# Optimization experiments

Measured on AMD Instinct MI355X. Metric: run time of the kernel, lower is better.

The kernel has to match this reference:

```python
import jax, jax.numpy as jnp
import numpy as np

B, N, C, H = 2, 2048, 1024, 16
D = C // H  # head_dim = 64


def setup_inputs() -> dict:
    key = jax.random.key(0)
    ks = jax.random.split(key, 5)
    s = 1.0 / np.sqrt(C)
    return {
        "q": jax.random.normal(ks[0], (B, N, C), dtype=jnp.float32),
        "W_qkv": jax.random.normal(ks[1], (C, 3 * C), dtype=jnp.float32) * s,
        "b_qkv": jnp.zeros((3 * C,), dtype=jnp.float32),
        "W_proj": jax.random.normal(ks[2], (C, C), dtype=jnp.float32) * s,
        "b_proj": jnp.zeros((C,), dtype=jnp.float32),
    }


def reference(q, W_qkv, b_qkv, W_proj, b_proj):
    # Self-attention: k = v = q. Full 3C projection (as in the torch code).
    qkv = q @ W_qkv + b_qkv  # [B, N, 3C]
    qh = qkv[:, :, :C].reshape(B, N, H, D)
    kh = qkv[:, :, C:2 * C].reshape(B, N, H, D)
    vh = qkv[:, :, 2 * C:].reshape(B, N, H, D)
    scale = D ** -0.5
    # [B, H, N, N] attention logits
    attn = jnp.einsum("bnhd,bmhd->bhnm", qh, kh) * scale
    attn = jax.nn.softmax(attn, axis=-1)
    out = jnp.einsum("bhnm,bmhd->bnhd", attn, vh).reshape(B, N, C)
    return out @ W_proj + b_proj
```

## Files before the change

kernel.cpp:

```cpp
#include <hip/hip_runtime.h>
#include <stdint.h>

typedef __bf16 bf16_t;
typedef __bf16 bf16x8 __attribute__((ext_vector_type(8)));
typedef __bf16 bf16x4 __attribute__((ext_vector_type(4)));
typedef float f32x4 __attribute__((ext_vector_type(4)));

#define L2E 1.44269504088896340736f
#define QSCALE (0.125f * L2E)

__device__ __forceinline__ void gload16(const bf16_t* g, bf16_t* l) {
  __builtin_amdgcn_global_load_lds(
      (const __attribute__((address_space(1))) void*)g,
      (__attribute__((address_space(3))) void*)l, 16, 0, 0);
}

__device__ __forceinline__ float fexp2(float x) {
  float r;
  asm("v_exp_f32 %0, %1" : "=v"(r) : "v"(x));
  return r;
}

__global__ __launch_bounds__(256) void cast_q_kernel(const float* __restrict__ in,
                                                     bf16_t* __restrict__ out) {
  int i = blockIdx.x * 256 + threadIdx.x;
  float4 v = reinterpret_cast<const float4*>(in)[i];
  bf16x4 o;
  o[0] = (bf16_t)v.x; o[1] = (bf16_t)v.y; o[2] = (bf16_t)v.z; o[3] = (bf16_t)v.w;
  reinterpret_cast<bf16x4*>(out)[i] = o;
}

__global__ __launch_bounds__(256) void transpose_cast_kernel(const float* __restrict__ in,
                                                             bf16_t* __restrict__ out,
                                                             int K, int N) {
  __shared__ float tile[64][65];
  int k0 = blockIdx.y * 64, n0 = blockIdx.x * 64;
  int t = threadIdx.x;
  int r = t >> 4, c4 = (t & 15) * 4;
#pragma unroll
  for (int rr = 0; rr < 4; rr++) {
    int row = r + rr * 16;
    float4 v = *reinterpret_cast<const float4*>(&in[(size_t)(k0 + row) * N + n0 + c4]);
    tile[row][c4 + 0] = v.x; tile[row][c4 + 1] = v.y;
    tile[row][c4 + 2] = v.z; tile[row][c4 + 3] = v.w;
  }
  __syncthreads();
#pragma unroll
  for (int rr = 0; rr < 4; rr++) {
    int nr = r + rr * 16;
    bf16x4 o;
#pragma unroll
    for (int i = 0; i < 4; i++) o[i] = (bf16_t)tile[c4 + i][nr];
    *reinterpret_cast<bf16x4*>(&out[(size_t)(n0 + nr) * K + k0 + c4]) = o;
  }
}

template <int MODE, int BM>
__global__ __launch_bounds__(256) void gemm_kernel(const bf16_t* __restrict__ A,
                                                   const bf16_t* __restrict__ Bt,
                                                   const float* __restrict__ bias,
                                                   void* __restrict__ out,
                                                   bf16_t* __restrict__ vT,
                                                   int K, int gm, int gn, int ldo) {
  constexpr int ACH = BM / 8;
  constexpr int NCH = ACH + 16;
  constexpr int CPW = NCH / 4;
  constexpr int IR = BM / 32;
  constexpr int SMEM = (MODE == 0) ? 17408 : (BM * 64 + 8192);
  __shared__ __align__(16) bf16_t smem[SMEM];
  bf16_t* At = smem;
  bf16_t* Bts = smem + BM * 64;
  const int t = threadIdx.x, lane = t & 63, w = t >> 6;
  const int g = lane >> 4, q = lane & 15;
  const int bid = blockIdx.x, x = bid & 7, r = bid >> 3;
  const int qm = gm >> 2, qn = gn >> 1;
  const int lm = r % qm, ln = r / qm;
  const int m0 = ((x & 3) * qm + lm) * BM, n0 = ((x >> 2) * qn + ln) * 128;
  const int wm = (w >> 1) * (BM / 2), wn = (w & 1) * 64;

  const bf16_t* srcp[CPW]; int dsto[CPW];
#pragma unroll
  for (int i = 0; i < CPW; i++) {
    int cI = i * 4 + w;
    bool isA = cI < ACH;
    int row = (isA ? cI : cI - ACH) * 8 + (lane >> 3);
    int p = (lane & 7) ^ (row & 7);
    srcp[i] = (isA ? A + (size_t)(m0 + row) * K : Bt + (size_t)(n0 + row) * K) + p * 8;
    dsto[i] = (isA ? cI * 512 : BM * 64 + (cI - ACH) * 512);
  }

  f32x4 acc[IR][4];
#pragma unroll
  for (int i = 0; i < IR; i++)
#pragma unroll
    for (int j = 0; j < 4; j++) acc[i][j] = (f32x4){0.f, 0.f, 0.f, 0.f};

  for (int k0 = 0; k0 < K; k0 += 64) {
    __syncthreads();
#pragma unroll
    for (int i = 0; i < CPW; i++) gload16(srcp[i] + k0, &smem[dsto[i]]);
    __syncthreads();
#pragma unroll
    for (int dc = 0; dc < 2; dc++) {
      bf16x8 am[IR], bn[4];
#pragma unroll
      for (int i = 0; i < IR; i++) {
        int ra = wm + 16 * i + q;
        am[i] = *reinterpret_cast<const bf16x8*>(&At[ra * 64 + ((dc * 32 + g * 8) ^ ((ra & 7) * 8))]);
      }
#pragma unroll
      for (int j = 0; j < 4; j++) {
        int rb = wn + 16 * j + q;
        bn[j] = *reinterpret_cast<const bf16x8*>(&Bts[rb * 64 + ((dc * 32 + g * 8) ^ ((rb & 7) * 8))]);
      }
#pragma unroll
      for (int i = 0; i < IR; i++)
#pragma unroll
        for (int j = 0; j < 4; j++)
          acc[i][j] = __builtin_amdgcn_mfma_f32_16x16x32_bf16(am[i], bn[j], acc[i][j], 0, 0, 0);
    }
  }

  if (MODE == 0 && n0 >= 2048) {
    __syncthreads();
    bf16_t* TT = smem;
#pragma unroll
    for (int i = 0; i < IR; i++)
#pragma unroll
      for (int j = 0; j < 4; j++)
#pragma unroll
        for (int rr = 0; rr < 4; rr++) {
          int ch = wn + 16 * j + q;
          int tok = wm + 16 * i + 4 * g + rr;
          float v = acc[i][j][rr] + bias[n0 + ch];
          TT[ch * 136 + (((tok >> 3) ^ (ch & 7)) * 8) + (tok & 7)] = (bf16_t)v;
        }
    __syncthreads();
    const int bb = m0 >> 11;
    const int t0 = m0 & 2047;
#pragma unroll
    for (int it = 0; it < 8; it++) {
      int ch = it * 16 + w * 4 + (lane >> 4);
      int ck = lane & 15;
      uint4 val = *reinterpret_cast<const uint4*>(&TT[ch * 136 + ((ck ^ (ch & 7)) * 8)]);
      int vch = (n0 - 2048) + ch;
      bf16_t* dst = vT + ((size_t)(bb * 16 + (vch >> 6)) * 64 + (vch & 63)) * 2048 + t0 + ck * 8;
      *reinterpret_cast<uint4*>(dst) = val;
    }
  } else {
#pragma unroll
    for (int i = 0; i < IR; i++)
#pragma unroll
      for (int j = 0; j < 4; j++)
#pragma unroll
        for (int rr = 0; rr < 4; rr++) {
          int row = m0 + wm + 16 * i + 4 * g + rr;
          int col = n0 + wn + 16 * j + q;
          float v = acc[i][j][rr] + bias[col];
          if (MODE == 0) {
            if (col < 1024) v *= QSCALE;
            ((bf16_t*)out)[(size_t)row * ldo + col] = (bf16_t)v;
          } else {
            ((float*)out)[(size_t)row * ldo + col] = v;
          }
        }
  }
}

__global__ __launch_bounds__(256) void attn_kernel(const bf16_t* __restrict__ qk,
                                                   const bf16_t* __restrict__ vT,
                                                   bf16_t* __restrict__ aout) {
  __shared__ __align__(16) bf16_t sK[2][4096];
  __shared__ __align__(16) bf16_t sV[2][4096];
  __shared__ __align__(16) bf16_t sP[4][1024];

  const int t = threadIdx.x, lane = t & 63, w = t >> 6;
  const int g = lane >> 4, q = lane & 15;
  const int bid = blockIdx.x, xr = bid >> 3;
  const int bh = (bid & 7) * 4 + (xr >> 5);
  const int b = bh >> 4, h = bh & 15;
  const int q0 = (xr & 31) * 64 + w * 16;
  const bf16_t* qk_b = qk + (size_t)b * 2048 * 2048;
  const bf16_t* vT_h = vT + (size_t)bh * 64 * 2048;
  bf16_t* Pw = sP[w];

  const bf16_t* srcK[2]; const bf16_t* srcV[2]; int dsto[2];
#pragma unroll
  for (int i = 0; i < 2; i++) {
    int gI = (w * 2 + i) * 64 + lane;
    int row = gI >> 3, p = (gI & 7) ^ (row & 7);
    srcK[i] = qk_b + (size_t)row * 2048 + 1024 + h * 64 + p * 8;
    srcV[i] = vT_h + (size_t)row * 2048 + p * 8;
    dsto[i] = (w * 2 + i) * 512;
  }

  bf16x8 bq[2];
  {
    const bf16_t* qr = qk_b + (size_t)(q0 + q) * 2048 + h * 64;
    bq[0] = *reinterpret_cast<const bf16x8*>(qr + g * 8);
    bq[1] = *reinterpret_cast<const bf16x8*>(qr + 32 + g * 8);
  }

  bf16x8 ones;
#pragma unroll
  for (int i = 0; i < 8; i++) ones[i] = (bf16_t)1.0f;

  f32x4 oacc[4];
#pragma unroll
  for (int c = 0; c < 4; c++) oacc[c] = (f32x4){0.f, 0.f, 0.f, 0.f};
  f32x4 lacc = (f32x4){0.f, 0.f, 0.f, 0.f};

#pragma unroll
  for (int i = 0; i < 2; i++) {
    gload16(srcK[i], &sK[0][dsto[i]]);
    gload16(srcV[i], &sV[0][dsto[i]]);
  }
  __syncthreads();

  for (int tt = 0; tt < 32; tt++) {
    const int cur = tt & 1;
    if (tt + 1 < 32) {
      size_t koffK = (size_t)(tt + 1) * 64 * 2048;
      size_t koffV = (size_t)(tt + 1) * 64;
#pragma unroll
      for (int i = 0; i < 2; i++) {
        gload16(srcK[i] + koffK, &sK[cur ^ 1][dsto[i]]);
        gload16(srcV[i] + koffV, &sV[cur ^ 1][dsto[i]]);
      }
    }

    const bf16_t* Kc = sK[cur];
    f32x4 s[4];
#pragma unroll
    for (int c = 0; c < 4; c++) {
      int row = 16 * c + q, sw = (q & 7) * 8;
      bf16x8 ka0 = *reinterpret_cast<const bf16x8*>(&Kc[row * 64 + ((g * 8) ^ sw)]);
      bf16x8 ka1 = *reinterpret_cast<const bf16x8*>(&Kc[row * 64 + ((32 + g * 8) ^ sw)]);
      f32x4 z = (f32x4){0.f, 0.f, 0.f, 0.f};
      z = __builtin_amdgcn_mfma_f32_16x16x32_bf16(ka0, bq[0], z, 0, 0, 0);
      z = __builtin_amdgcn_mfma_f32_16x16x32_bf16(ka1, bq[1], z, 0, 0, 0);
      s[c] = z;
    }

#pragma unroll
    for (int c = 0; c < 4; c++) {
      bf16x4 pk;
#pragma unroll
      for (int rr = 0; rr < 4; rr++) pk[rr] = (bf16_t)fexp2(s[c][rr]);
      *reinterpret_cast<bf16x4*>(
          &Pw[q * 64 + (((2 * c + (g >> 1)) ^ (q & 7)) * 8) + (g & 1) * 4]) = pk;
    }

    const bf16_t* Vc = sV[cur];
#pragma unroll
    for (int kc = 0; kc < 2; kc++) {
      bf16x8 pb = *reinterpret_cast<const bf16x8*>(
          &Pw[q * 64 + (((kc * 4 + g) ^ (q & 7)) * 8)]);
      lacc = __builtin_amdgcn_mfma_f32_16x16x32_bf16(ones, pb, lacc, 0, 0, 0);
#pragma unroll
      for (int c = 0; c < 4; c++) {
        int row = 16 * c + q;
        bf16x8 va = *reinterpret_cast<const bf16x8*>(
            &Vc[row * 64 + (((kc * 4 + g) ^ (q & 7)) * 8)]);
        oacc[c] = __builtin_amdgcn_mfma_f32_16x16x32_bf16(va, pb, oacc[c], 0, 0, 0);
      }
    }

    __syncthreads();
  }

  float inv = 1.0f / lacc[0];
  bf16_t* orow = aout + (size_t)(b * 2048 + q0 + q) * 1024 + h * 64;
#pragma unroll
  for (int c = 0; c < 4; c++) {
    bf16x4 ov;
#pragma unroll
    for (int rr = 0; rr < 4; rr++) ov[rr] = (bf16_t)(oacc[c][rr] * inv);
    *reinterpret_cast<bf16x4*>(orow + c * 16 + g * 4) = ov;
  }
}

extern "C" void kernel_launch(void* const* d_in, const int* in_sizes, int n_in,
                              void* d_out, int out_size, void* d_ws, size_t ws_size,
                              hipStream_t stream) {
  const float* q     = (const float*)d_in[0];
  const float* Wqkv  = (const float*)d_in[1];
  const float* bqkv  = (const float*)d_in[2];
  const float* Wproj = (const float*)d_in[3];
  const float* bproj = (const float*)d_in[4];
  float* out = (float*)d_out;

  char* ws = (char*)d_ws;
  bf16_t* q_bf    = (bf16_t*)(ws);
  bf16_t* wqkv_t  = (bf16_t*)(ws + 8388608);
  bf16_t* wproj_t = (bf16_t*)(ws + 14680064);
  bf16_t* qk      = (bf16_t*)(ws + 16777216);
  bf16_t* vT      = (bf16_t*)(ws + 33554432);
  bf16_t* aout    = q_bf;

  cast_q_kernel<<<4096, 256, 0, stream>>>(q, q_bf);
  transpose_cast_kernel<<<dim3(48, 16), 256, 0, stream>>>(Wqkv, wqkv_t, 1024, 3072);
  transpose_cast_kernel<<<dim3(16, 16), 256, 0, stream>>>(Wproj, wproj_t, 1024, 1024);
  gemm_kernel<0, 128><<<768, 256, 0, stream>>>(q_bf, wqkv_t, bqkv, qk, vT, 1024, 32, 24, 2048);
  attn_kernel<<<1024, 256, 0, stream>>>(qk, vT, aout);
  gemm_kernel<1, 64><<<512, 256, 0, stream>>>(aout, wproj_t, bproj, out, nullptr, 1024, 64, 8, 1024);
}
```

Before: 134.5 us.

## Rewrite attention with 32x32x16 MFMA and register-resident P via lane shuffles

The attention kernel now uses 32x32x16 bf16 MFMA tiles. Each of 2 waves per block handles 32 query rows instead of 4 waves handling 16 rows each. The softmax probabilities are packed to bf16 and exchanged between half-waves with __shfl_xor instead of being staged through shared memory. The row sum is accumulated in scalar registers rather than with an extra MFMA against a ones vector. This removes the LDS round trip for P and the redundant ones-MFMA, and gives fewer, larger MFMAs. In exchange there are fewer waves per block, so latency hiding may suffer, and register pressure is higher.

Measured after the change: 142.2 us. 5.7% more time.

```diff
diff --git a/kernel.cpp b/kernel.cpp
--- a/kernel.cpp
+++ b/kernel.cpp
@@ -5,6 +5,7 @@
 typedef __bf16 bf16x8 __attribute__((ext_vector_type(8)));
 typedef __bf16 bf16x4 __attribute__((ext_vector_type(4)));
 typedef float f32x4 __attribute__((ext_vector_type(4)));
+typedef float f32x16 __attribute__((ext_vector_type(16)));
 
 #define L2E 1.44269504088896340736f
 #define QSCALE (0.125f * L2E)
@@ -19,6 +20,12 @@
   float r;
   asm("v_exp_f32 %0, %1" : "=v"(r) : "v"(x));
   return r;
+}
+
+__device__ __forceinline__ unsigned packbf2(float a, float b) {
+  union { __bf16 h[2]; unsigned u; } x;
+  x.h[0] = (bf16_t)a; x.h[1] = (bf16_t)b;
+  return x.u;
 }
 
 __global__ __launch_bounds__(256) void cast_q_kernel(const float* __restrict__ in,
@@ -167,51 +174,46 @@
   }
 }
 
-__global__ __launch_bounds__(256) void attn_kernel(const bf16_t* __restrict__ qk,
+__global__ __launch_bounds__(128) void attn_kernel(const bf16_t* __restrict__ qk,
                                                    const bf16_t* __restrict__ vT,
                                                    bf16_t* __restrict__ aout) {
   __shared__ __align__(16) bf16_t sK[2][4096];
   __shared__ __align__(16) bf16_t sV[2][4096];
-  __shared__ __align__(16) bf16_t sP[4][1024];
 
   const int t = threadIdx.x, lane = t & 63, w = t >> 6;
-  const int g = lane >> 4, q = lane & 15;
+  const int l31 = lane & 31, hl = lane >> 5;
   const int bid = blockIdx.x, xr = bid >> 3;
   const int bh = (bid & 7) * 4 + (xr >> 5);
-  const int b = bh >> 4, h = bh & 15;
-  const int q0 = (xr & 31) * 64 + w * 16;
+  const int b = bh >> 4, hd = bh & 15;
+  const int q0 = (xr & 31) * 64 + w * 32;
   const bf16_t* qk_b = qk + (size_t)b * 2048 * 2048;
   const bf16_t* vT_h = vT + (size_t)bh * 64 * 2048;
-  bf16_t* Pw = sP[w];
-
-  const bf16_t* srcK[2]; const bf16_t* srcV[2]; int dsto[2];
-#pragma unroll
-  for (int i = 0; i < 2; i++) {
-    int gI = (w * 2 + i) * 64 + lane;
+
+  const bf16_t* srcK[4]; const bf16_t* srcV[4]; int dsto[4];
+#pragma unroll
+  for (int i = 0; i < 4; i++) {
+    int gI = (w * 4 + i) * 64 + lane;
     int row = gI >> 3, p = (gI & 7) ^ (row & 7);
-    srcK[i] = qk_b + (size_t)row * 2048 + 1024 + h * 64 + p * 8;
+    srcK[i] = qk_b + (size_t)row * 2048 + 1024 + hd * 64 + p * 8;
     srcV[i] = vT_h + (size_t)row * 2048 + p * 8;
-    dsto[i] = (w * 2 + i) * 512;
-  }
-
-  bf16x8 bq[2];
+    dsto[i] = (w * 4 + i) * 512;
+  }
+
+  bf16x8 bq[4];
   {
-    const bf16_t* qr = qk_b + (size_t)(q0 + q) * 2048 + h * 64;
-    bq[0] = *reinterpret_cast<const bf16x8*>(qr + g * 8);
-    bq[1] = *reinterpret_cast<const bf16x8*>(qr + 32 + g * 8);
-  }
-
-  bf16x8 ones;
-#pragma unroll
-  for (int i = 0; i < 8; i++) ones[i] = (bf16_t)1.0f;
-
-  f32x4 oacc[4];
-#pragma unroll
-  for (int c = 0; c < 4; c++) oacc[c] = (f32x4){0.f, 0.f, 0.f, 0.f};
-  f32x4 lacc = (f32x4){0.f, 0.f, 0.f, 0.f};
-
-#pragma unroll
-  for (int i = 0; i < 2; i++) {
+    const bf16_t* qr = qk_b + (size_t)(q0 + l31) * 2048 + hd * 64;
+#pragma unroll
+    for (int ks = 0; ks < 4; ks++)
+      bq[ks] = *reinterpret_cast<const bf16x8*>(qr + hl * 8 + 16 * ks);
+  }
+
+  f32x16 oacc0 = {0.f}, oacc1 = {0.f};
+#pragma unroll
+  for (int r = 0; r < 16; r++) { oacc0[r] = 0.f; oacc1[r] = 0.f; }
+  float psum = 0.f;
+
+#pragma unroll
+  for (int i = 0; i < 4; i++) {
     gload16(srcK[i], &sK[0][dsto[i]]);
     gload16(srcV[i], &sV[0][dsto[i]]);
   }
@@ -223,60 +225,76 @@
       size_t koffK = (size_t)(tt + 1) * 64 * 2048;
       size_t koffV = (size_t)(tt + 1) * 64;
 #pragma unroll
-      for (int i = 0; i < 2; i++) {
+      for (int i = 0; i < 4; i++) {
         gload16(srcK[i] + koffK, &sK[cur ^ 1][dsto[i]]);
         gload16(srcV[i] + koffV, &sV[cur ^ 1][dsto[i]]);
       }
     }
 
     const bf16_t* Kc = sK[cur];
-    f32x4 s[4];
-#pragma unroll
-    for (int c = 0; c < 4; c++) {
-      int row = 16 * c + q, sw = (q & 7) * 8;
-      bf16x8 ka0 = *reinterpret_cast<const bf16x8*>(&Kc[row * 64 + ((g * 8) ^ sw)]);
-      bf16x8 ka1 = *reinterpret_cast<const bf16x8*>(&Kc[row * 64 + ((32 + g * 8) ^ sw)]);
-      f32x4 z = (f32x4){0.f, 0.f, 0.f, 0.f};
-      z = __builtin_amdgcn_mfma_f32_16x16x32_bf16(ka0, bq[0], z, 0, 0, 0);
-      z = __builtin_amdgcn_mfma_f32_16x16x32_bf16(ka1, bq[1], z, 0, 0, 0);
-      s[c] = z;
-    }
-
-#pragma unroll
-    for (int c = 0; c < 4; c++) {
-      bf16x4 pk;
-#pragma unroll
-      for (int rr = 0; rr < 4; rr++) pk[rr] = (bf16_t)fexp2(s[c][rr]);
-      *reinterpret_cast<bf16x4*>(
-          &Pw[q * 64 + (((2 * c + (g >> 1)) ^ (q & 7)) * 8) + (g & 1) * 4]) = pk;
-    }
-
     const bf16_t* Vc = sV[cur];
-#pragma unroll
-    for (int kc = 0; kc < 2; kc++) {
-      bf16x8 pb = *reinterpret_cast<const bf16x8*>(
-          &Pw[q * 64 + (((kc * 4 + g) ^ (q & 7)) * 8)]);
-      lacc = __builtin_amdgcn_mfma_f32_16x16x32_bf16(ones, pb, lacc, 0, 0, 0);
-#pragma unroll
-      for (int c = 0; c < 4; c++) {
-        int row = 16 * c + q;
-        bf16x8 va = *reinterpret_cast<const bf16x8*>(
-            &Vc[row * 64 + (((kc * 4 + g) ^ (q & 7)) * 8)]);
-        oacc[c] = __builtin_amdgcn_mfma_f32_16x16x32_bf16(va, pb, oacc[c], 0, 0, 0);
-      }
-    }
-
-    __syncthreads();
-  }
-
-  float inv = 1.0f / lacc[0];
-  bf16_t* orow = aout + (size_t)(b * 2048 + q0 + q) * 1024 + h * 64;
-#pragma unroll
-  for (int c = 0; c < 4; c++) {
-    bf16x4 ov;
-#pragma unroll
-    for (int rr = 0; rr < 4; rr++) ov[rr] = (bf16_t)(oacc[c][rr] * inv);
-    *reinterpret_cast<bf16x4*>(orow + c * 16 + g * 4) = ov;
+    const int sw = l31 & 7;
+
+    f32x16 sb0, sb1;
+#pragma unroll
+    for (int r = 0; r < 16; r++) { sb0[r] = 0.f; sb1[r] = 0.f; }
+#pragma unroll
+    for (int ks = 0; ks < 4; ks++) {
+      int ch = ((hl + 2 * ks) ^ sw) * 8;
+      bf16x8 ka0 = *reinterpret_cast<const bf16x8*>(&Kc[l31 * 64 + ch]);
+      bf16x8 ka1 = *reinterpret_cast<const bf16x8*>(&Kc[(32 + l31) * 64 + ch]);
+      sb0 = __builtin_amdgcn_mfma_f32_32x32x16_bf16(ka0, bq[ks], sb0, 0, 0, 0);
+      sb1 = __builtin_amdgcn_mfma_f32_32x32x16_bf16(ka1, bq[ks], sb1, 0, 0, 0);
+    }
+
+    unsigned pk0[8], pk1[8];
+#pragma unroll
+    for (int m = 0; m < 8; m++) {
+      float a0 = fexp2(sb0[2 * m]), b0 = fexp2(sb0[2 * m + 1]);
+      float a1 = fexp2(sb1[2 * m]), b1 = fexp2(sb1[2 * m + 1]);
+      psum += (a0 + b0) + (a1 + b1);
+      pk0[m] = packbf2(a0, b0);
+      pk1[m] = packbf2(a1, b1);
+    }
+
+#pragma unroll
+    for (int S = 0; S < 4; S++) {
+      const int s_ = S & 1;
+      unsigned X0, X1, Y0, Y1;
+      if (S < 2) { X0 = pk0[4 * s_ + 0]; X1 = pk0[4 * s_ + 1]; Y0 = pk0[4 * s_ + 2]; Y1 = pk0[4 * s_ + 3]; }
+      else       { X0 = pk1[4 * s_ + 0]; X1 = pk1[4 * s_ + 1]; Y0 = pk1[4 * s_ + 2]; Y1 = pk1[4 * s_ + 3]; }
+      unsigned Xx0 = (unsigned)__shfl_xor((int)X0, 32);
+      unsigned Yx0 = (unsigned)__shfl_xor((int)Y0, 32);
+      unsigned Xx1 = (unsigned)__shfl_xor((int)X1, 32);
+      unsigned Yx1 = (unsigned)__shfl_xor((int)Y1, 32);
+      union { unsigned u[4]; bf16x8 v; } pb;
+      pb.u[0] = hl ? Yx0 : X0;
+      pb.u[1] = hl ? Yx1 : X1;
+      pb.u[2] = hl ? Y0 : Xx0;
+      pb.u[3] = hl ? Y1 : Xx1;
+      int ch = ((2 * S + hl) ^ sw) * 8;
+      bf16x8 va0 = *reinterpret_cast<const bf16x8*>(&Vc[l31 * 64 + ch]);
+      bf16x8 va1 = *reinterpret_cast<const bf16x8*>(&Vc[(32 + l31) * 64 + ch]);
+      oacc0 = __builtin_amdgcn_mfma_f32_32x32x16_bf16(va0, pb.v, oacc0, 0, 0, 0);
+      oacc1 = __builtin_amdgcn_mfma_f32_32x32x16_bf16(va1, pb.v, oacc1, 0, 0, 0);
+    }
+
+    __syncthreads();
+  }
+
+  psum += __shfl_xor(psum, 32);
+  float inv = 1.0f / psum;
+  bf16_t* orow = aout + (size_t)(b * 2048 + q0 + l31) * 1024 + hd * 64;
+#pragma unroll
+  for (int k = 0; k < 4; k++) {
+    bf16x4 ov0, ov1;
+#pragma unroll
+    for (int r = 0; r < 4; r++) {
+      ov0[r] = (bf16_t)(oacc0[4 * k + r] * inv);
+      ov1[r] = (bf16_t)(oacc1[4 * k + r] * inv);
+    }
+    *reinterpret_cast<bf16x4*>(orow + 8 * k + 4 * hl) = ov0;
+    *reinterpret_cast<bf16x4*>(orow + 32 + 8 * k + 4 * hl) = ov1;
   }
 }
 
@@ -302,6 +320,6 @@
   transpose_cast_kernel<<<dim3(48, 16), 256, 0, stream>>>(Wqkv, wqkv_t, 1024, 3072);
   transpose_cast_kernel<<<dim3(16, 16), 256, 0, stream>>>(Wproj, wproj_t, 1024, 1024);
   gemm_kernel<0, 128><<<768, 256, 0, stream>>>(q_bf, wqkv_t, bqkv, qk, vT, 1024, 32, 24, 2048);
-  attn_kernel<<<1024, 256, 0, stream>>>(qk, vT, aout);
+  attn_kernel<<<1024, 128, 0, stream>>>(qk, vT, aout);
   gemm_kernel<1, 64><<<512, 256, 0, stream>>>(aout, wproj_t, bproj, out, nullptr, 1024, 64, 8, 1024);
 }
```
